# Performance work log

Hardware: AMD Instinct MI355X
Metric: run time of the kernel (lower is better)

## Reference

```python
import jax, jax.numpy as jnp
import numpy as np

DIM = 384; HEADS = 6; K = 10; G = 2
GC = DIM // G            # group channel dim
HD = DIM // HEADS        # head dim
SCALE = HD ** -0.5
LN_EPS = 1e-5


def _sqdist(a, b):
    # a: [..., n, 3], b: [..., m, 3] -> [..., n, m]
    return (jnp.sum(a * a, -1)[..., :, None]
            + jnp.sum(b * b, -1)[..., None, :]
            - 2.0 * jnp.einsum('...nc,...mc->...nm', a, b))


def setup_inputs() -> dict:
    key = jax.random.key(0)
    ks = jax.random.split(key, 12)
    B, N, M = 4, 1024, 1024
    s = 0.02
    return {
        'q': jax.random.normal(ks[0], (B, N, DIM), jnp.float32),
        'q_pos': jax.random.normal(ks[1], (B, N, 3), jnp.float32),
        'v': jax.random.normal(ks[2], (B, M, DIM), jnp.float32),
        'v_pos': jax.random.normal(ks[3], (B, M, 3), jnp.float32),
        'Wq': jax.random.normal(ks[4], (DIM, DIM), jnp.float32) * s,
        'Wk': jax.random.normal(ks[5], (DIM, DIM), jnp.float32) * s,
        'Wv': jax.random.normal(ks[6], (DIM, DIM), jnp.float32) * s,
        'Wvoff': jax.random.normal(ks[7], (DIM, DIM), jnp.float32) * s,
        'Woff1': jax.random.normal(ks[8], (DIM, 2 * GC), jnp.float32) * s,
        'boff1': jnp.zeros((DIM,), jnp.float32),
        'ln_g': jnp.ones((DIM,), jnp.float32),
        'ln_b': jnp.zeros((DIM,), jnp.float32),
        'Woff2': jax.random.normal(ks[9], (3, DIM), jnp.float32) * s,
        'Wproj': jax.random.normal(ks[10], (DIM, DIM), jnp.float32) * s,
        'bproj': jnp.zeros((DIM,), jnp.float32),
    }


def reference(q, q_pos, v, v_pos, Wq, Wk, Wv, Wvoff, Woff1, boff1,
              ln_g, ln_b, Woff2, Wproj, bproj):
    B, N, C = q.shape
    M = v.shape[1]

    # --- knn_point: K nearest v_pos for each q_pos ---
    idx = jax.lax.top_k(-_sqdist(q_pos, v_pos), K)[1]        # [B,N,K]
    idx_flat = idx.reshape(B, N * K, 1)

    qp = q @ Wq.T                                            # [B,N,C]
    v_off = v @ Wvoff.T                                      # [B,M,C]

    # index_points gathers
    local_v = jnp.take_along_axis(v_off, idx_flat, axis=1).reshape(B, N, K, C)
    local_v_pos = jnp.take_along_axis(v_pos, idx_flat, axis=1).reshape(B, N, K, 3)

    # group split: 'b n k (g c) -> b g n k c'
    off_local_v = local_v.reshape(B, N, K, G, GC).transpose(0, 3, 1, 2, 4)  # [B,G,N,K,GC]
    group_q = qp.reshape(B, N, G, GC).transpose(0, 2, 1, 3)                 # [B,G,N,GC]

    shift_feat = jnp.concatenate(
        [off_local_v, jnp.broadcast_to(group_q[:, :, :, None, :], (B, G, N, K, GC))], -1)

    # linear_offset MLP: Linear -> LayerNorm -> GELU(exact) -> Linear, then tanh
    h = shift_feat @ Woff1.T + boff1                          # [B,G,N,K,DIM]
    mu = h.mean(-1, keepdims=True)
    var = h.var(-1, keepdims=True)
    h = (h - mu) / jnp.sqrt(var + LN_EPS) * ln_g + ln_b
    h = jax.nn.gelu(h, approximate=False)
    offset = jnp.tanh(h @ Woff2.T)                            # [B,G,N,K,3]

    shift_pos = (local_v_pos[:, None] + offset).reshape(B, G, N * K, 3)
    vg = v.reshape(B, M, G, GC).transpose(0, 2, 1, 3)         # [B,G,M,GC]

    # --- three_nn + reciprocal-distance three_interpolate ---
    sqd = _sqdist(shift_pos, v_pos[:, None])                  # [B,G,N*K,M]
    negd, idx3 = jax.lax.top_k(-sqd, 3)                       # 3 smallest
    dist = jnp.sqrt(jnp.maximum(-negd, 0.0))                  # [B,G,N*K,3]
    w = 1.0 / (dist + 1e-8)
    w = w / jnp.sum(w, -1, keepdims=True)
    feats = jnp.take_along_axis(vg, idx3.reshape(B, G, N * K * 3, 1), axis=2)
    feats = feats.reshape(B, G, N * K, 3, GC)
    interp = jnp.einsum('bgnj,bgnjc->bgnc', w, feats)         # [B,G,N*K,GC]
    # '(b g) (n k) c -> b n k (g c)'
    interp = interp.reshape(B, G, N, K, GC).transpose(0, 2, 3, 1, 4).reshape(B, N, K, C)

    # --- local cross-attention (each query attends to its K interpolated feats) ---
    kf = (interp @ Wk.T).reshape(B, N, K, HEADS, HD)
    vf = (interp @ Wv.T).reshape(B, N, K, HEADS, HD)
    qh = qp.reshape(B, N, HEADS, HD)
    attn = jnp.einsum('bnhd,bnkhd->bhnk', qh, kf) * SCALE
    attn = jax.nn.softmax(attn, axis=-1)
    out = jnp.einsum('bhnk,bnkhd->bnhd', attn, vf).reshape(B, N, C)
    return out @ Wproj.T + bproj
```

## Files before the change

kernel.cpp:

```cpp
#include <hip/hip_runtime.h>
#include <math.h>

#define NB 4
#define NN 1024
#define NM 1024
#define NC 384
#define NK 10
#define NG 2
#define NGC 192
#define NH 6

#define GSZ ((size_t)NB * NM * NC)
#define QSZ ((size_t)NB * NN * NC)
#define NCNC ((size_t)NC * NC)

#define OFF_WQ 0
#define OFF_W1B 147456
#define OFF_WK0 221184
#define OFF_WK1 294912
#define OFF_WV0 368640
#define OFF_WV1 442368
#define OFF_WPROJ 516096
#define WT_ALL_FLOATS 663552

__device__ __forceinline__ float wred_sum(float v) {
#pragma unroll
  for (int m = 32; m >= 1; m >>= 1) v += __shfl_xor(v, m, 64);
  return v;
}

__device__ __forceinline__ void wred_argmin(float& d, int& m) {
#pragma unroll
  for (int off = 32; off >= 1; off >>= 1) {
    float od = __shfl_xor(d, off, 64);
    int om = __shfl_xor(m, off, 64);
    if (od < d || (od == d && om < m)) { d = od; m = om; }
  }
}

__device__ __forceinline__ ushort f2bf(float x) {
  unsigned u = __float_as_uint(x);
  unsigned r = (u + 0x7fffu + ((u >> 16) & 1u)) >> 16;
  return (ushort)r;
}
__device__ __forceinline__ float b2f(ushort s) {
  return __uint_as_float(((unsigned)s) << 16);
}

__global__ void transpose_all_k(const float* __restrict__ Wq, const float* __restrict__ Woff1,
                                const float* __restrict__ Wk, const float* __restrict__ Wv,
                                const float* __restrict__ Wproj, float* __restrict__ Wt_all) {
  const float* W;
  int i0, icount, doff;
  switch (blockIdx.y) {
    case 0: W = Wq;    i0 = 0;   icount = NC;  doff = OFF_WQ;    break;
    case 1: W = Woff1; i0 = NGC; icount = NGC; doff = OFF_W1B;   break;
    case 2: W = Wk;    i0 = 0;   icount = NGC; doff = OFF_WK0;   break;
    case 3: W = Wk;    i0 = NGC; icount = NGC; doff = OFF_WK1;   break;
    case 4: W = Wv;    i0 = 0;   icount = NGC; doff = OFF_WV0;   break;
    case 5: W = Wv;    i0 = NGC; icount = NGC; doff = OFF_WV1;   break;
    default: W = Wproj; i0 = 0;  icount = NC;  doff = OFF_WPROJ; break;
  }
  int id = blockIdx.x * 256 + threadIdx.x;
  if (id >= icount * NC) return;
  int o = id % NC;
  int i = id / NC;
  Wt_all[doff + (size_t)i * NC + o] = W[(size_t)o * NC + i0 + i];
}

__global__ __launch_bounds__(256) void wcomb2_k(const float* __restrict__ Woff1,
                                                const float* __restrict__ Wvoff,
                                                const float* __restrict__ Wq,
                                                float* __restrict__ WcombAll) {
  int o = blockIdx.x;
  int job = blockIdx.y;
  int g = job & 1, kind = job >> 1;
  const float* Wsrc = kind ? Wq : Wvoff;
  __shared__ float w1[NGC];
  for (int j = threadIdx.x; j < NGC; j += 256) w1[j] = Woff1[(size_t)o * NC + kind * NGC + j];
  __syncthreads();
  for (int i = threadIdx.x; i < NC; i += 256) {
    float acc = 0.f;
#pragma unroll 4
    for (int j = 0; j < NGC; ++j)
      acc = fmaf(w1[j], Wsrc[(size_t)(g * NGC + j) * NC + i], acc);
    WcombAll[((size_t)job * NC + i) * NC + o] = acc;
  }
}

__global__ __launch_bounds__(384) void gemm16_k(const float* __restrict__ X, int IN, int xoff0,
                                                int xoff_stride, const float* __restrict__ Wt0,
                                                size_t wstride, const float* __restrict__ bias,
                                                float* __restrict__ Y0, size_t ystride) {
  __shared__ __align__(16) float xs[NC][20];
  int tid = threadIdx.x;
  int og = tid % 96, rg = tid / 96;
  int r0 = blockIdx.x * 16;
  int job = blockIdx.y;
  int xoff = xoff0 + job * xoff_stride;
  const float* Wt = Wt0 + (size_t)job * wstride;
  float* Y = Y0 + (size_t)job * ystride;
  for (int t = tid; t < 16 * IN; t += 384) {
    int r = t / IN, kk = t % IN;
    xs[kk][r] = X[(size_t)(r0 + r) * NC + xoff + kk];
  }
  __syncthreads();
  float acc[4][4];
#pragma unroll
  for (int i = 0; i < 4; ++i)
#pragma unroll
    for (int j = 0; j < 4; ++j) acc[i][j] = 0.f;
  int o = og * 4;
#pragma unroll 4
  for (int kk = 0; kk < IN; ++kk) {
    float4 w4 = *(const float4*)&Wt[(size_t)kk * NC + o];
    float4 x4 = *(const float4*)&xs[kk][rg * 4];
    float xr[4] = {x4.x, x4.y, x4.z, x4.w};
    float wr[4] = {w4.x, w4.y, w4.z, w4.w};
#pragma unroll
    for (int ri = 0; ri < 4; ++ri)
#pragma unroll
      for (int oi = 0; oi < 4; ++oi) acc[ri][oi] = fmaf(xr[ri], wr[oi], acc[ri][oi]);
  }
  float4 bv = make_float4(0.f, 0.f, 0.f, 0.f);
  if (bias) bv = *(const float4*)&bias[o];
#pragma unroll
  for (int ri = 0; ri < 4; ++ri) {
    float4 ov;
    ov.x = acc[ri][0] + bv.x;
    ov.y = acc[ri][1] + bv.y;
    ov.z = acc[ri][2] + bv.z;
    ov.w = acc[ri][3] + bv.w;
    *(float4*)&Y[(size_t)(r0 + rg * 4 + ri) * NC + o] = ov;
  }
}

__global__ __launch_bounds__(384) void projall_k(const float* __restrict__ q,
                                                 const float* __restrict__ v,
                                                 const float* __restrict__ WcombAll,
                                                 const float* __restrict__ Wt_all,
                                                 float* __restrict__ qp,
                                                 float* __restrict__ qcontrib,
                                                 float* __restrict__ vcontrib,
                                                 ushort* __restrict__ KcT,
                                                 ushort* __restrict__ VcT) {
  __shared__ __align__(16) float xs[NC][20];
  int tid = threadIdx.x;
  int og = tid % 96, rg = tid / 96;
  int r0 = blockIdx.x * 16;
  int job = blockIdx.y;
  const float* X;
  const float* Wt;
  int IN, xoff;
  float* Yf = nullptr;
  ushort* Yh = nullptr;
  switch (job) {
    case 0: X = v; IN = NC;  xoff = 0;   Wt = WcombAll;            Yf = vcontrib;       break;
    case 1: X = v; IN = NC;  xoff = 0;   Wt = WcombAll + NCNC;     Yf = vcontrib + GSZ; break;
    case 2: X = v; IN = NGC; xoff = 0;   Wt = Wt_all + OFF_WK0;    Yh = KcT;            break;
    case 3: X = v; IN = NGC; xoff = NGC; Wt = Wt_all + OFF_WK1;    Yh = KcT + GSZ;      break;
    case 4: X = v; IN = NGC; xoff = 0;   Wt = Wt_all + OFF_WV0;    Yh = VcT;            break;
    case 5: X = v; IN = NGC; xoff = NGC; Wt = Wt_all + OFF_WV1;    Yh = VcT + GSZ;      break;
    case 6: X = q; IN = NC;  xoff = 0;   Wt = Wt_all + OFF_WQ;     Yf = qp;             break;
    case 7: X = q; IN = NC;  xoff = 0;   Wt = WcombAll + 2 * NCNC; Yf = qcontrib;       break;
    default:X = q; IN = NC;  xoff = 0;   Wt = WcombAll + 3 * NCNC; Yf = qcontrib + QSZ; break;
  }
  for (int t = tid; t < 16 * IN; t += 384) {
    int r = t / IN, kk = t % IN;
    xs[kk][r] = X[(size_t)(r0 + r) * NC + xoff + kk];
  }
  __syncthreads();
  float acc[4][4];
#pragma unroll
  for (int i = 0; i < 4; ++i)
#pragma unroll
    for (int j = 0; j < 4; ++j) acc[i][j] = 0.f;
  int o = og * 4;
#pragma unroll 4
  for (int kk = 0; kk < IN; ++kk) {
    float4 w4 = *(const float4*)&Wt[(size_t)kk * NC + o];
    float4 x4 = *(const float4*)&xs[kk][rg * 4];
    float xr[4] = {x4.x, x4.y, x4.z, x4.w};
    float wr[4] = {w4.x, w4.y, w4.z, w4.w};
#pragma unroll
    for (int ri = 0; ri < 4; ++ri)
#pragma unroll
      for (int oi = 0; oi < 4; ++oi) acc[ri][oi] = fmaf(xr[ri], wr[oi], acc[ri][oi]);
  }
  if (Yf) {
#pragma unroll
    for (int ri = 0; ri < 4; ++ri)
      *(float4*)&Yf[(size_t)(r0 + rg * 4 + ri) * NC + o] =
          make_float4(acc[ri][0], acc[ri][1], acc[ri][2], acc[ri][3]);
  } else {
#pragma unroll
    for (int ri = 0; ri < 4; ++ri) {
      ushort4 pk;
      pk.x = f2bf(acc[ri][0]);
      pk.y = f2bf(acc[ri][1]);
      pk.z = f2bf(acc[ri][2]);
      pk.w = f2bf(acc[ri][3]);
      *(ushort4*)&Yh[(size_t)(r0 + rg * 4 + ri) * NC + o] = pk;
    }
  }
}

__global__ __launch_bounds__(256) void knn2_k(const float* __restrict__ q_pos,
                                              const float* __restrict__ v_pos,
                                              int* __restrict__ knn_idx) {
  __shared__ float4 cpos[NM];
  int tid = threadIdx.x, lane = tid & 63, wid = tid >> 6;
  int b = blockIdx.x / (NN / 4);
  int n = (blockIdx.x % (NN / 4)) * 4 + wid;
  for (int t = tid; t < NM; t += 256) {
    float x = v_pos[((size_t)b * NM + t) * 3 + 0];
    float y = v_pos[((size_t)b * NM + t) * 3 + 1];
    float z = v_pos[((size_t)b * NM + t) * 3 + 2];
    cpos[t] = make_float4(x, y, z, x * x + y * y + z * z);
  }
  __syncthreads();
  float qx = q_pos[((size_t)b * NN + n) * 3 + 0];
  float qy = q_pos[((size_t)b * NN + n) * 3 + 1];
  float qz = q_pos[((size_t)b * NN + n) * 3 + 2];
  float qq = qx * qx + qy * qy + qz * qz;
  float bd[NK];
  int bi[NK];
#pragma unroll
  for (int j = 0; j < NK; ++j) { bd[j] = 1e30f; bi[j] = 0x7fffffff; }
#pragma unroll
  for (int t = 0; t < NM / 64; ++t) {
    int m = t * 64 + lane;
    float4 cc = cpos[m];
    float d = qq + cc.w - 2.f * (qx * cc.x + qy * cc.y + qz * cc.z);
    if (d < bd[NK - 1]) {
#pragma unroll
      for (int j = NK - 1; j > 0; --j) {
        if (d < bd[j - 1]) { bd[j] = bd[j - 1]; bi[j] = bi[j - 1]; }
        else if (d < bd[j]) { bd[j] = d; bi[j] = m; }
      }
      if (d < bd[0]) { bd[0] = d; bi[0] = m; }
    }
  }
  size_t base = ((size_t)b * NN + n) * NK;
#pragma unroll
  for (int round = 0; round < NK; ++round) {
    float dh = bd[0];
    int mh = bi[0];
    wred_argmin(dh, mh);
    if (lane == 0) knn_idx[base + round] = mh;
    if (bi[0] == mh) {
#pragma unroll
      for (int j = 0; j < NK - 1; ++j) { bd[j] = bd[j + 1]; bi[j] = bi[j + 1]; }
      bd[NK - 1] = 1e30f; bi[NK - 1] = 0x7fffffff;
    }
  }
}

__global__ __launch_bounds__(256) void mlp3nn_k(
    const float* __restrict__ vcontrib, const float* __restrict__ qcontrib,
    const float* __restrict__ boff1, const float* __restrict__ ln_g,
    const float* __restrict__ ln_b, const float* __restrict__ Woff2,
    const int* __restrict__ knn_idx, const float* __restrict__ v_pos,
    int* __restrict__ idx3, float* __restrict__ w3) {
  __shared__ float4 cpos[NM];
  int tid = threadIdx.x, lane = tid & 63, wid = tid >> 6;
  int r = blockIdx.x * 4 + wid;
  int b = (blockIdx.x * 4) / (NK * NN * NG);
  for (int t = tid; t < NM; t += 256) {
    float x = v_pos[((size_t)b * NM + t) * 3 + 0];
    float y = v_pos[((size_t)b * NM + t) * 3 + 1];
    float z = v_pos[((size_t)b * NM + t) * 3 + 2];
    cpos[t] = make_float4(x, y, z, x * x + y * y + z * z);
  }
  __syncthreads();
  int k = r % NK;
  int n = (r / NK) % NN;
  int g = (r / (NK * NN)) % NG;
  int m = knn_idx[((size_t)b * NN + n) * NK + k];
  const float* vc = vcontrib + ((size_t)(g * NB + b) * NM + m) * NC;
  const float* qc = qcontrib + ((size_t)(g * NB + b) * NN + n) * NC;
  float h[6];
  float s = 0.f, s2 = 0.f;
#pragma unroll
  for (int j = 0; j < 6; ++j) {
    int c = j * 64 + lane;
    float x = vc[c] + qc[c] + boff1[c];
    h[j] = x; s += x; s2 += x * x;
  }
  s = wred_sum(s);
  s2 = wred_sum(s2);
  float mean = s * (1.f / NC);
  float var = s2 * (1.f / NC) - mean * mean;
  float inv = 1.f / sqrtf(var + 1e-5f);
  float p0 = 0.f, p1 = 0.f, p2 = 0.f;
#pragma unroll
  for (int j = 0; j < 6; ++j) {
    int c = j * 64 + lane;
    float x = (h[j] - mean) * inv * ln_g[c] + ln_b[c];
    x = 0.5f * x * (1.f + erff(x * 0.70710678118654752f));
    p0 = fmaf(x, Woff2[0 * NC + c], p0);
    p1 = fmaf(x, Woff2[1 * NC + c], p1);
    p2 = fmaf(x, Woff2[2 * NC + c], p2);
  }
  p0 = wred_sum(p0);
  p1 = wred_sum(p1);
  p2 = wred_sum(p2);
  float4 cm = cpos[m];
  float sx = cm.x + tanhf(p0);
  float sy = cm.y + tanhf(p1);
  float sz = cm.z + tanhf(p2);
  float qq2 = sx * sx + sy * sy + sz * sz;
  float d0v = 1e30f, d1v = 1e30f, d2v = 1e30f;
  int i0v = 0x7fffffff, i1v = 0x7fffffff, i2v = 0x7fffffff;
#pragma unroll
  for (int t = 0; t < NM / 64; ++t) {
    int m2 = t * 64 + lane;
    float4 cc = cpos[m2];
    float d = qq2 + cc.w - 2.f * (sx * cc.x + sy * cc.y + sz * cc.z);
    if (d < d2v) {
      d2v = d; i2v = m2;
      if (d2v < d1v) { float td = d1v; d1v = d2v; d2v = td; int ti = i1v; i1v = i2v; i2v = ti; }
      if (d1v < d0v) { float td = d0v; d0v = d1v; d1v = td; int ti = i0v; i0v = i1v; i1v = ti; }
    }
  }
  float rd[3];
  int rm[3];
#pragma unroll
  for (int round = 0; round < 3; ++round) {
    float dh = d0v;
    int mh = i0v;
    wred_argmin(dh, mh);
    rd[round] = dh; rm[round] = mh;
    if (i0v == mh) {
      d0v = d1v; i0v = i1v;
      d1v = d2v; i1v = i2v;
      d2v = 1e30f; i2v = 0x7fffffff;
    }
  }
  if (lane == 0) {
    float e0 = 1.f / (sqrtf(fmaxf(rd[0], 0.f)) + 1e-8f);
    float e1 = 1.f / (sqrtf(fmaxf(rd[1], 0.f)) + 1e-8f);
    float e2 = 1.f / (sqrtf(fmaxf(rd[2], 0.f)) + 1e-8f);
    float sw = e0 + e1 + e2;
    idx3[(size_t)r * 3 + 0] = rm[0]; w3[(size_t)r * 3 + 0] = e0 / sw;
    idx3[(size_t)r * 3 + 1] = rm[1]; w3[(size_t)r * 3 + 1] = e1 / sw;
    idx3[(size_t)r * 3 + 2] = rm[2]; w3[(size_t)r * 3 + 2] = e2 / sw;
  }
}

__global__ __launch_bounds__(NC) void attn_k(const float* __restrict__ qp,
                                             const ushort* __restrict__ Kc,
                                             const ushort* __restrict__ Vc,
                                             const int* __restrict__ idx3,
                                             const float* __restrict__ w3,
                                             float* __restrict__ attn_out) {
  __shared__ float vfs[NK][NC];
  __shared__ float lgs[NH][NK];
  __shared__ int il[NG][NK][3];
  __shared__ float wl[NG][NK][3];
  int o = threadIdx.x;
  int lane = o & 63, wid = o >> 6;
  int b = blockIdx.x / NN;
  int n = blockIdx.x % NN;
  if (o < NG * NK * 3) {
    int g = o / (NK * 3), k = (o / 3) % NK, j = o % 3;
    size_t rr = (((size_t)(b * NG + g) * NN + n) * NK + k) * 3 + j;
    il[g][k][j] = idx3[rr];
    wl[g][k][j] = w3[rr];
  }
  __syncthreads();
  float qv = qp[((size_t)b * NN + n) * NC + o];
  for (int k = 0; k < NK; ++k) {
    float kf = 0.f, vf = 0.f;
#pragma unroll
    for (int g = 0; g < NG; ++g)
#pragma unroll
      for (int j = 0; j < 3; ++j) {
        int m = il[g][k][j];
        float w = wl[g][k][j];
        size_t base = ((size_t)(g * NB + b) * NM + m) * NC + o;
        kf = fmaf(w, b2f(Kc[base]), kf);
        vf = fmaf(w, b2f(Vc[base]), vf);
      }
    vfs[k][o] = vf;
    float p = wred_sum(qv * kf);
    if (lane == 0) lgs[wid][k] = p * 0.125f;
  }
  __syncthreads();
  float a[NK];
  float mx = -1e30f;
#pragma unroll
  for (int k = 0; k < NK; ++k) { a[k] = lgs[wid][k]; mx = fmaxf(mx, a[k]); }
  float sum = 0.f;
#pragma unroll
  for (int k = 0; k < NK; ++k) { a[k] = expf(a[k] - mx); sum += a[k]; }
  float outv = 0.f;
#pragma unroll
  for (int k = 0; k < NK; ++k) outv = fmaf(a[k] / sum, vfs[k][o], outv);
  attn_out[((size_t)b * NN + n) * NC + o] = outv;
}

extern "C" void kernel_launch(void* const* d_in, const int* in_sizes, int n_in,
                              void* d_out, int out_size, void* d_ws, size_t ws_size,
                              hipStream_t stream) {
  (void)in_sizes; (void)n_in; (void)out_size; (void)ws_size;
  const float* q     = (const float*)d_in[0];
  const float* q_pos = (const float*)d_in[1];
  const float* v     = (const float*)d_in[2];
  const float* v_pos = (const float*)d_in[3];
  const float* Wq    = (const float*)d_in[4];
  const float* Wk    = (const float*)d_in[5];
  const float* Wv    = (const float*)d_in[6];
  const float* Wvoff = (const float*)d_in[7];
  const float* Woff1 = (const float*)d_in[8];
  const float* boff1 = (const float*)d_in[9];
  const float* ln_g  = (const float*)d_in[10];
  const float* ln_b  = (const float*)d_in[11];
  const float* Woff2 = (const float*)d_in[12];
  const float* Wproj = (const float*)d_in[13];
  const float* bproj = (const float*)d_in[14];
  float* out = (float*)d_out;

  char* p = (char*)d_ws;
  auto alloc_f = [&](size_t n) { float* r = (float*)p; p += n * sizeof(float); return r; };
  auto alloc_h = [&](size_t n) { ushort* r = (ushort*)p; p += n * sizeof(ushort); return r; };
  auto alloc_i = [&](size_t n) { int* r = (int*)p; p += n * sizeof(int); return r; };

  float* qp        = alloc_f(QSZ);
  float* qcontrib  = alloc_f((size_t)NG * QSZ);
  float* vcontrib  = alloc_f((size_t)NG * GSZ);
  float* Wt_all    = alloc_f((size_t)WT_ALL_FLOATS);
  float* WcombAll  = alloc_f((size_t)4 * NCNC);
  float* w3        = alloc_f((size_t)NB * NG * NN * NK * 3);
  ushort* KcT      = alloc_h((size_t)NG * GSZ);
  ushort* VcT      = alloc_h((size_t)NG * GSZ);
  int* knn_idx     = alloc_i((size_t)NB * NN * NK);
  int* idx3        = alloc_i((size_t)NB * NG * NN * NK * 3);
  float* attn_out  = vcontrib;

  transpose_all_k<<<dim3(576, 7), 256, 0, stream>>>(Wq, Woff1, Wk, Wv, Wproj, Wt_all);
  wcomb2_k<<<dim3(NC, 4), 256, 0, stream>>>(Woff1, Wvoff, Wq, WcombAll);
  knn2_k<<<NB * (NN / 4), 256, 0, stream>>>(q_pos, v_pos, knn_idx);

  projall_k<<<dim3(NB * NM / 16, 9), 384, 0, stream>>>(q, v, WcombAll, Wt_all, qp, qcontrib,
                                                       vcontrib, KcT, VcT);

  mlp3nn_k<<<NB * NG * NN * NK / 4, 256, 0, stream>>>(vcontrib, qcontrib, boff1, ln_g, ln_b,
                                                      Woff2, knn_idx, v_pos, idx3, w3);
  attn_k<<<NB * NN, NC, 0, stream>>>(qp, KcT, VcT, idx3, w3, attn_out);
  gemm16_k<<<dim3(NB * NN / 16, 1), 384, 0, stream>>>(attn_out, NC, 0, 0, Wt_all + OFF_WPROJ, 0,
                                                      bproj, out, 0);
}
```

Before: 497.7 us.

## Unify GEMMs into 32-row K-chunked kernel and derive qcontrib from qp

Replaces the 16-row projection and output GEMM kernels with a single 32-row-tile kernel that stages the input through shared memory in 96-wide K chunks. Each thread now computes 8x4 outputs, which doubles reuse of every weight load. The q-side offset contributions are now computed from the already projected qp through the transposed Woff1 block, replacing the precombined Woff1·Wq matrices. This halves the Wcomb precompute work but adds an extra dependent launch. The output projection reuses the same kernel, and the larger accumulator tile raises register pressure.

```diff
diff --git a/kernel.cpp b/kernel.cpp
--- a/kernel.cpp
+++ b/kernel.cpp
@@ -68,139 +68,98 @@
   Wt_all[doff + (size_t)i * NC + o] = W[(size_t)o * NC + i0 + i];
 }
 
-__global__ __launch_bounds__(256) void wcomb2_k(const float* __restrict__ Woff1,
-                                                const float* __restrict__ Wvoff,
-                                                const float* __restrict__ Wq,
-                                                float* __restrict__ WcombAll) {
+__global__ void wcomb_k(const float* __restrict__ Woff1, const float* __restrict__ Wvoff,
+                        float* __restrict__ Wcomb_t) {
   int o = blockIdx.x;
-  int job = blockIdx.y;
-  int g = job & 1, kind = job >> 1;
-  const float* Wsrc = kind ? Wq : Wvoff;
+  int g = blockIdx.y;
+  int i = threadIdx.x;
   __shared__ float w1[NGC];
-  for (int j = threadIdx.x; j < NGC; j += 256) w1[j] = Woff1[(size_t)o * NC + kind * NGC + j];
+  if (i < NGC) w1[i] = Woff1[(size_t)o * NC + i];
   __syncthreads();
-  for (int i = threadIdx.x; i < NC; i += 256) {
-    float acc = 0.f;
+  float acc = 0.f;
 #pragma unroll 4
-    for (int j = 0; j < NGC; ++j)
-      acc = fmaf(w1[j], Wsrc[(size_t)(g * NGC + j) * NC + i], acc);
-    WcombAll[((size_t)job * NC + i) * NC + o] = acc;
-  }
-}
-
-__global__ __launch_bounds__(384) void gemm16_k(const float* __restrict__ X, int IN, int xoff0,
-                                                int xoff_stride, const float* __restrict__ Wt0,
-                                                size_t wstride, const float* __restrict__ bias,
-                                                float* __restrict__ Y0, size_t ystride) {
-  __shared__ __align__(16) float xs[NC][20];
+  for (int j = 0; j < NGC; ++j)
+    acc = fmaf(w1[j], Wvoff[(size_t)(g * NGC + j) * NC + i], acc);
+  Wcomb_t[((size_t)g * NC + i) * NC + o] = acc;
+}
+
+__global__ __launch_bounds__(384, 2) void gemm32_k(
+    int jobbase, const float* __restrict__ q, const float* __restrict__ v,
+    const float* __restrict__ qp_in, const float* __restrict__ attn_in,
+    const float* __restrict__ Wcomb_t, const float* __restrict__ Wt_all,
+    const float* __restrict__ bproj, float* __restrict__ qp,
+    float* __restrict__ qcontrib, float* __restrict__ vcontrib,
+    ushort* __restrict__ KcT, ushort* __restrict__ VcT, float* __restrict__ outp) {
+  __shared__ __align__(16) float xs[96][36];
   int tid = threadIdx.x;
   int og = tid % 96, rg = tid / 96;
-  int r0 = blockIdx.x * 16;
-  int job = blockIdx.y;
-  int xoff = xoff0 + job * xoff_stride;
-  const float* Wt = Wt0 + (size_t)job * wstride;
-  float* Y = Y0 + (size_t)job * ystride;
-  for (int t = tid; t < 16 * IN; t += 384) {
-    int r = t / IN, kk = t % IN;
-    xs[kk][r] = X[(size_t)(r0 + r) * NC + xoff + kk];
-  }
-  __syncthreads();
-  float acc[4][4];
-#pragma unroll
-  for (int i = 0; i < 4; ++i)
-#pragma unroll
-    for (int j = 0; j < 4; ++j) acc[i][j] = 0.f;
   int o = og * 4;
-#pragma unroll 4
-  for (int kk = 0; kk < IN; ++kk) {
-    float4 w4 = *(const float4*)&Wt[(size_t)kk * NC + o];
-    float4 x4 = *(const float4*)&xs[kk][rg * 4];
-    float xr[4] = {x4.x, x4.y, x4.z, x4.w};
-    float wr[4] = {w4.x, w4.y, w4.z, w4.w};
-#pragma unroll
-    for (int ri = 0; ri < 4; ++ri)
-#pragma unroll
-      for (int oi = 0; oi < 4; ++oi) acc[ri][oi] = fmaf(xr[ri], wr[oi], acc[ri][oi]);
-  }
-  float4 bv = make_float4(0.f, 0.f, 0.f, 0.f);
-  if (bias) bv = *(const float4*)&bias[o];
-#pragma unroll
-  for (int ri = 0; ri < 4; ++ri) {
-    float4 ov;
-    ov.x = acc[ri][0] + bv.x;
-    ov.y = acc[ri][1] + bv.y;
-    ov.z = acc[ri][2] + bv.z;
-    ov.w = acc[ri][3] + bv.w;
-    *(float4*)&Y[(size_t)(r0 + rg * 4 + ri) * NC + o] = ov;
-  }
-}
-
-__global__ __launch_bounds__(384) void projall_k(const float* __restrict__ q,
-                                                 const float* __restrict__ v,
-                                                 const float* __restrict__ WcombAll,
-                                                 const float* __restrict__ Wt_all,
-                                                 float* __restrict__ qp,
-                                                 float* __restrict__ qcontrib,
-                                                 float* __restrict__ vcontrib,
-                                                 ushort* __restrict__ KcT,
-                                                 ushort* __restrict__ VcT) {
-  __shared__ __align__(16) float xs[NC][20];
-  int tid = threadIdx.x;
-  int og = tid % 96, rg = tid / 96;
-  int r0 = blockIdx.x * 16;
-  int job = blockIdx.y;
+  int r0 = blockIdx.x * 32;
+  int job = jobbase + blockIdx.y;
   const float* X;
   const float* Wt;
   int IN, xoff;
   float* Yf = nullptr;
   ushort* Yh = nullptr;
+  const float* bias = nullptr;
   switch (job) {
-    case 0: X = v; IN = NC;  xoff = 0;   Wt = WcombAll;            Yf = vcontrib;       break;
-    case 1: X = v; IN = NC;  xoff = 0;   Wt = WcombAll + NCNC;     Yf = vcontrib + GSZ; break;
-    case 2: X = v; IN = NGC; xoff = 0;   Wt = Wt_all + OFF_WK0;    Yh = KcT;            break;
-    case 3: X = v; IN = NGC; xoff = NGC; Wt = Wt_all + OFF_WK1;    Yh = KcT + GSZ;      break;
-    case 4: X = v; IN = NGC; xoff = 0;   Wt = Wt_all + OFF_WV0;    Yh = VcT;            break;
-    case 5: X = v; IN = NGC; xoff = NGC; Wt = Wt_all + OFF_WV1;    Yh = VcT + GSZ;      break;
-    case 6: X = q; IN = NC;  xoff = 0;   Wt = Wt_all + OFF_WQ;     Yf = qp;             break;
-    case 7: X = q; IN = NC;  xoff = 0;   Wt = WcombAll + 2 * NCNC; Yf = qcontrib;       break;
-    default:X = q; IN = NC;  xoff = 0;   Wt = WcombAll + 3 * NCNC; Yf = qcontrib + QSZ; break;
-  }
-  for (int t = tid; t < 16 * IN; t += 384) {
-    int r = t / IN, kk = t % IN;
-    xs[kk][r] = X[(size_t)(r0 + r) * NC + xoff + kk];
-  }
-  __syncthreads();
-  float acc[4][4];
-#pragma unroll
-  for (int i = 0; i < 4; ++i)
+    case 0: X = v;       IN = NC;  xoff = 0;   Wt = Wcomb_t;           Yf = vcontrib;       break;
+    case 1: X = v;       IN = NC;  xoff = 0;   Wt = Wcomb_t + NCNC;    Yf = vcontrib + GSZ; break;
+    case 2: X = v;       IN = NGC; xoff = 0;   Wt = Wt_all + OFF_WK0;  Yh = KcT;            break;
+    case 3: X = v;       IN = NGC; xoff = NGC; Wt = Wt_all + OFF_WK1;  Yh = KcT + GSZ;      break;
+    case 4: X = v;       IN = NGC; xoff = 0;   Wt = Wt_all + OFF_WV0;  Yh = VcT;            break;
+    case 5: X = v;       IN = NGC; xoff = NGC; Wt = Wt_all + OFF_WV1;  Yh = VcT + GSZ;      break;
+    case 6: X = q;       IN = NC;  xoff = 0;   Wt = Wt_all + OFF_WQ;   Yf = qp;             break;
+    case 7: X = qp_in;   IN = NGC; xoff = 0;   Wt = Wt_all + OFF_W1B;  Yf = qcontrib;       break;
+    case 8: X = qp_in;   IN = NGC; xoff = NGC; Wt = Wt_all + OFF_W1B;  Yf = qcontrib + QSZ; break;
+    default: X = attn_in; IN = NC; xoff = 0;   Wt = Wt_all + OFF_WPROJ; Yf = outp; bias = bproj; break;
+  }
+  float acc[8][4];
+#pragma unroll
+  for (int i = 0; i < 8; ++i)
 #pragma unroll
     for (int j = 0; j < 4; ++j) acc[i][j] = 0.f;
-  int o = og * 4;
+  for (int kc = 0; kc < IN; kc += 96) {
+    for (int t = tid; t < 32 * 96; t += 384) {
+      int r = t / 96, kk = t % 96;
+      xs[kk][r] = X[(size_t)(r0 + r) * NC + xoff + kc + kk];
+    }
+    __syncthreads();
 #pragma unroll 4
-  for (int kk = 0; kk < IN; ++kk) {
-    float4 w4 = *(const float4*)&Wt[(size_t)kk * NC + o];
-    float4 x4 = *(const float4*)&xs[kk][rg * 4];
-    float xr[4] = {x4.x, x4.y, x4.z, x4.w};
-    float wr[4] = {w4.x, w4.y, w4.z, w4.w};
-#pragma unroll
-    for (int ri = 0; ri < 4; ++ri)
-#pragma unroll
-      for (int oi = 0; oi < 4; ++oi) acc[ri][oi] = fmaf(xr[ri], wr[oi], acc[ri][oi]);
-  }
+    for (int kk = 0; kk < 96; ++kk) {
+      float4 w4 = *(const float4*)&Wt[(size_t)(kc + kk) * NC + o];
+      float4 xa = *(const float4*)&xs[kk][rg * 8];
+      float4 xb = *(const float4*)&xs[kk][rg * 8 + 4];
+      float xr[8] = {xa.x, xa.y, xa.z, xa.w, xb.x, xb.y, xb.z, xb.w};
+      float wr[4] = {w4.x, w4.y, w4.z, w4.w};
+#pragma unroll
+      for (int ri = 0; ri < 8; ++ri)
+#pragma unroll
+        for (int oi = 0; oi < 4; ++oi) acc[ri][oi] = fmaf(xr[ri], wr[oi], acc[ri][oi]);
+    }
+    __syncthreads();
+  }
+  float4 bv = make_float4(0.f, 0.f, 0.f, 0.f);
+  if (bias) bv = *(const float4*)&bias[o];
   if (Yf) {
 #pragma unroll
-    for (int ri = 0; ri < 4; ++ri)
-      *(float4*)&Yf[(size_t)(r0 + rg * 4 + ri) * NC + o] =
-          make_float4(acc[ri][0], acc[ri][1], acc[ri][2], acc[ri][3]);
+    for (int ri = 0; ri < 8; ++ri) {
+      float4 ov;
+      ov.x = acc[ri][0] + bv.x;
+      ov.y = acc[ri][1] + bv.y;
+      ov.z = acc[ri][2] + bv.z;
+      ov.w = acc[ri][3] + bv.w;
+      *(float4*)&Yf[(size_t)(r0 + rg * 8 + ri) * NC + o] = ov;
+    }
   } else {
 #pragma unroll
-    for (int ri = 0; ri < 4; ++ri) {
+    for (int ri = 0; ri < 8; ++ri) {
       ushort4 pk;
       pk.x = f2bf(acc[ri][0]);
       pk.y = f2bf(acc[ri][1]);
       pk.z = f2bf(acc[ri][2]);
       pk.w = f2bf(acc[ri][3]);
-      *(ushort4*)&Yh[(size_t)(r0 + rg * 4 + ri) * NC + o] = pk;
+      *(ushort4*)&Yh[(size_t)(r0 + rg * 8 + ri) * NC + o] = pk;
     }
   }
 }
@@ -430,7 +389,7 @@
   float* qcontrib  = alloc_f((size_t)NG * QSZ);
   float* vcontrib  = alloc_f((size_t)NG * GSZ);
   float* Wt_all    = alloc_f((size_t)WT_ALL_FLOATS);
-  float* WcombAll  = alloc_f((size_t)4 * NCNC);
+  float* Wcomb_t   = alloc_f((size_t)NG * NCNC);
   float* w3        = alloc_f((size_t)NB * NG * NN * NK * 3);
   ushort* KcT      = alloc_h((size_t)NG * GSZ);
   ushort* VcT      = alloc_h((size_t)NG * GSZ);
@@ -439,15 +398,20 @@
   float* attn_out  = vcontrib;
 
   transpose_all_k<<<dim3(576, 7), 256, 0, stream>>>(Wq, Woff1, Wk, Wv, Wproj, Wt_all);
-  wcomb2_k<<<dim3(NC, 4), 256, 0, stream>>>(Woff1, Wvoff, Wq, WcombAll);
+  wcomb_k<<<dim3(NC, NG), NC, 0, stream>>>(Woff1, Wvoff, Wcomb_t);
   knn2_k<<<NB * (NN / 4), 256, 0, stream>>>(q_pos, v_pos, knn_idx);
 
-  projall_k<<<dim3(NB * NM / 16, 9), 384, 0, stream>>>(q, v, WcombAll, Wt_all, qp, qcontrib,
-                                                       vcontrib, KcT, VcT);
+  gemm32_k<<<dim3(NB * NM / 32, 7), 384, 0, stream>>>(0, q, v, qp, attn_out, Wcomb_t, Wt_all,
+                                                      bproj, qp, qcontrib, vcontrib, KcT, VcT,
+                                                      out);
+  gemm32_k<<<dim3(NB * NN / 32, 2), 384, 0, stream>>>(7, q, v, qp, attn_out, Wcomb_t, Wt_all,
+                                                      bproj, qp, qcontrib, vcontrib, KcT, VcT,
+                                                      out);
 
   mlp3nn_k<<<NB * NG * NN * NK / 4, 256, 0, stream>>>(vcontrib, qcontrib, boff1, ln_g, ln_b,
                                                       Woff2, knn_idx, v_pos, idx3, w3);
   attn_k<<<NB * NN, NC, 0, stream>>>(qp, KcT, VcT, idx3, w3, attn_out);
-  gemm16_k<<<dim3(NB * NN / 16, 1), 384, 0, stream>>>(attn_out, NC, 0, 0, Wt_all + OFF_WPROJ, 0,
-                                                      bproj, out, 0);
-}
+  gemm32_k<<<dim3(NB * NN / 32, 1), 384, 0, stream>>>(9, q, v, qp, attn_out, Wcomb_t, Wt_all,
+                                                      bproj, qp, qcontrib, vcontrib, KcT, VcT,
+                                                      out);
+}
```

Measured after the change: 510.1 us. 1.02x slower.

## Compute q-side offset contribution from qp instead of fused Wq weights; register-reduce attention

Applied to the files above, without the earlier changes.

The q-side offset contributions are no longer computed with precombined Woff1·Wq matrices over 384 inputs. They are now obtained by first computing qp and then applying the 192-wide Woff1 slice, which halves the inner dimension for those two GEMMs and drops two weight-combination jobs. The cost is an extra dependent launch, since qp must finish before qcontrib. The attention kernel also keeps the per-key logits and values in registers, reducing all ten logits with butterfly shuffles instead of shared memory plus a block barrier.

```diff
diff --git a/kernel.cpp b/kernel.cpp
--- a/kernel.cpp
+++ b/kernel.cpp
@@ -68,24 +68,19 @@
   Wt_all[doff + (size_t)i * NC + o] = W[(size_t)o * NC + i0 + i];
 }
 
-__global__ __launch_bounds__(256) void wcomb2_k(const float* __restrict__ Woff1,
-                                                const float* __restrict__ Wvoff,
-                                                const float* __restrict__ Wq,
-                                                float* __restrict__ WcombAll) {
+__global__ void wcomb_k(const float* __restrict__ Woff1, const float* __restrict__ Wvoff,
+                        float* __restrict__ Wcomb_t) {
   int o = blockIdx.x;
-  int job = blockIdx.y;
-  int g = job & 1, kind = job >> 1;
-  const float* Wsrc = kind ? Wq : Wvoff;
+  int g = blockIdx.y;
+  int i = threadIdx.x;
   __shared__ float w1[NGC];
-  for (int j = threadIdx.x; j < NGC; j += 256) w1[j] = Woff1[(size_t)o * NC + kind * NGC + j];
-  __syncthreads();
-  for (int i = threadIdx.x; i < NC; i += 256) {
-    float acc = 0.f;
+  if (i < NGC) w1[i] = Woff1[(size_t)o * NC + i];
+  __syncthreads();
+  float acc = 0.f;
 #pragma unroll 4
-    for (int j = 0; j < NGC; ++j)
-      acc = fmaf(w1[j], Wsrc[(size_t)(g * NGC + j) * NC + i], acc);
-    WcombAll[((size_t)job * NC + i) * NC + o] = acc;
-  }
+  for (int j = 0; j < NGC; ++j)
+    acc = fmaf(w1[j], Wvoff[(size_t)(g * NGC + j) * NC + i], acc);
+  Wcomb_t[((size_t)g * NC + i) * NC + o] = acc;
 }
 
 __global__ __launch_bounds__(384) void gemm16_k(const float* __restrict__ X, int IN, int xoff0,
@@ -135,39 +130,32 @@
   }
 }
 
-__global__ __launch_bounds__(384) void projall_k(const float* __restrict__ q,
-                                                 const float* __restrict__ v,
-                                                 const float* __restrict__ WcombAll,
-                                                 const float* __restrict__ Wt_all,
-                                                 float* __restrict__ qp,
-                                                 float* __restrict__ qcontrib,
-                                                 float* __restrict__ vcontrib,
-                                                 ushort* __restrict__ KcT,
-                                                 ushort* __restrict__ VcT) {
+__global__ __launch_bounds__(384) void vproj_k(const float* __restrict__ v,
+                                               const float* __restrict__ Wcomb_t,
+                                               const float* __restrict__ Wt_all,
+                                               float* __restrict__ vcontrib,
+                                               ushort* __restrict__ KcT,
+                                               ushort* __restrict__ VcT) {
   __shared__ __align__(16) float xs[NC][20];
   int tid = threadIdx.x;
   int og = tid % 96, rg = tid / 96;
   int r0 = blockIdx.x * 16;
   int job = blockIdx.y;
-  const float* X;
   const float* Wt;
-  int IN, xoff;
   float* Yf = nullptr;
   ushort* Yh = nullptr;
+  int IN, xoff;
   switch (job) {
-    case 0: X = v; IN = NC;  xoff = 0;   Wt = WcombAll;            Yf = vcontrib;       break;
-    case 1: X = v; IN = NC;  xoff = 0;   Wt = WcombAll + NCNC;     Yf = vcontrib + GSZ; break;
-    case 2: X = v; IN = NGC; xoff = 0;   Wt = Wt_all + OFF_WK0;    Yh = KcT;            break;
-    case 3: X = v; IN = NGC; xoff = NGC; Wt = Wt_all + OFF_WK1;    Yh = KcT + GSZ;      break;
-    case 4: X = v; IN = NGC; xoff = 0;   Wt = Wt_all + OFF_WV0;    Yh = VcT;            break;
-    case 5: X = v; IN = NGC; xoff = NGC; Wt = Wt_all + OFF_WV1;    Yh = VcT + GSZ;      break;
-    case 6: X = q; IN = NC;  xoff = 0;   Wt = Wt_all + OFF_WQ;     Yf = qp;             break;
-    case 7: X = q; IN = NC;  xoff = 0;   Wt = WcombAll + 2 * NCNC; Yf = qcontrib;       break;
-    default:X = q; IN = NC;  xoff = 0;   Wt = WcombAll + 3 * NCNC; Yf = qcontrib + QSZ; break;
+    case 0: Wt = Wcomb_t;        IN = NC;  xoff = 0;   Yf = vcontrib;       break;
+    case 1: Wt = Wcomb_t + NCNC; IN = NC;  xoff = 0;   Yf = vcontrib + GSZ; break;
+    case 2: Wt = Wt_all + OFF_WK0; IN = NGC; xoff = 0;   Yh = KcT;          break;
+    case 3: Wt = Wt_all + OFF_WK1; IN = NGC; xoff = NGC; Yh = KcT + GSZ;    break;
+    case 4: Wt = Wt_all + OFF_WV0; IN = NGC; xoff = 0;   Yh = VcT;          break;
+    default: Wt = Wt_all + OFF_WV1; IN = NGC; xoff = NGC; Yh = VcT + GSZ;   break;
   }
   for (int t = tid; t < 16 * IN; t += 384) {
     int r = t / IN, kk = t % IN;
-    xs[kk][r] = X[(size_t)(r0 + r) * NC + xoff + kk];
+    xs[kk][r] = v[(size_t)(r0 + r) * NC + xoff + kk];
   }
   __syncthreads();
   float acc[4][4];
@@ -354,12 +342,9 @@
                                              const int* __restrict__ idx3,
                                              const float* __restrict__ w3,
                                              float* __restrict__ attn_out) {
-  __shared__ float vfs[NK][NC];
-  __shared__ float lgs[NH][NK];
   __shared__ int il[NG][NK][3];
   __shared__ float wl[NG][NK][3];
   int o = threadIdx.x;
-  int lane = o & 63, wid = o >> 6;
   int b = blockIdx.x / NN;
   int n = blockIdx.x % NN;
   if (o < NG * NK * 3) {
@@ -370,8 +355,10 @@
   }
   __syncthreads();
   float qv = qp[((size_t)b * NN + n) * NC + o];
+  float p[NK], vf[NK];
+#pragma unroll
   for (int k = 0; k < NK; ++k) {
-    float kf = 0.f, vf = 0.f;
+    float kf = 0.f, v_ = 0.f;
 #pragma unroll
     for (int g = 0; g < NG; ++g)
 #pragma unroll
@@ -380,23 +367,26 @@
         float w = wl[g][k][j];
         size_t base = ((size_t)(g * NB + b) * NM + m) * NC + o;
         kf = fmaf(w, b2f(Kc[base]), kf);
-        vf = fmaf(w, b2f(Vc[base]), vf);
+        v_ = fmaf(w, b2f(Vc[base]), v_);
       }
-    vfs[k][o] = vf;
-    float p = wred_sum(qv * kf);
-    if (lane == 0) lgs[wid][k] = p * 0.125f;
-  }
-  __syncthreads();
+    vf[k] = v_;
+    p[k] = qv * kf;
+  }
+#pragma unroll
+  for (int off = 32; off >= 1; off >>= 1) {
+#pragma unroll
+    for (int k = 0; k < NK; ++k) p[k] += __shfl_xor(p[k], off, 64);
+  }
   float a[NK];
   float mx = -1e30f;
 #pragma unroll
-  for (int k = 0; k < NK; ++k) { a[k] = lgs[wid][k]; mx = fmaxf(mx, a[k]); }
+  for (int k = 0; k < NK; ++k) { a[k] = p[k] * 0.125f; mx = fmaxf(mx, a[k]); }
   float sum = 0.f;
 #pragma unroll
   for (int k = 0; k < NK; ++k) { a[k] = expf(a[k] - mx); sum += a[k]; }
   float outv = 0.f;
 #pragma unroll
-  for (int k = 0; k < NK; ++k) outv = fmaf(a[k] / sum, vfs[k][o], outv);
+  for (int k = 0; k < NK; ++k) outv = fmaf(a[k] / sum, vf[k], outv);
   attn_out[((size_t)b * NN + n) * NC + o] = outv;
 }
 
@@ -430,7 +420,7 @@
   float* qcontrib  = alloc_f((size_t)NG * QSZ);
   float* vcontrib  = alloc_f((size_t)NG * GSZ);
   float* Wt_all    = alloc_f((size_t)WT_ALL_FLOATS);
-  float* WcombAll  = alloc_f((size_t)4 * NCNC);
+  float* Wcomb_t   = alloc_f((size_t)NG * NCNC);
   float* w3        = alloc_f((size_t)NB * NG * NN * NK * 3);
   ushort* KcT      = alloc_h((size_t)NG * GSZ);
   ushort* VcT      = alloc_h((size_t)NG * GSZ);
@@ -439,11 +429,14 @@
   float* attn_out  = vcontrib;
 
   transpose_all_k<<<dim3(576, 7), 256, 0, stream>>>(Wq, Woff1, Wk, Wv, Wproj, Wt_all);
-  wcomb2_k<<<dim3(NC, 4), 256, 0, stream>>>(Woff1, Wvoff, Wq, WcombAll);
+  wcomb_k<<<dim3(NC, NG), NC, 0, stream>>>(Woff1, Wvoff, Wcomb_t);
+
+  gemm16_k<<<dim3(NB * NN / 16, 1), 384, 0, stream>>>(q, NC, 0, 0, Wt_all + OFF_WQ, 0, nullptr,
+                                                      qp, 0);
   knn2_k<<<NB * (NN / 4), 256, 0, stream>>>(q_pos, v_pos, knn_idx);
-
-  projall_k<<<dim3(NB * NM / 16, 9), 384, 0, stream>>>(q, v, WcombAll, Wt_all, qp, qcontrib,
-                                                       vcontrib, KcT, VcT);
+  gemm16_k<<<dim3(NB * NN / 16, 2), 384, 0, stream>>>(qp, NGC, 0, NGC, Wt_all + OFF_W1B, 0,
+                                                      nullptr, qcontrib, QSZ);
+  vproj_k<<<dim3(NB * NM / 16, 6), 384, 0, stream>>>(v, Wcomb_t, Wt_all, vcontrib, KcT, VcT);
 
   mlp3nn_k<<<NB * NG * NN * NK / 4, 256, 0, stream>>>(vcontrib, qcontrib, boff1, ln_g, ln_b,
                                                       Woff2, knn_idx, v_pos, idx3, w3);
```

New measurement: 530.7 us. 1.07x slower.
